# Performance work log

Hardware: AMD Instinct MI355X
Metric: run time of the kernel (lower is better)

The kernel has to match this reference:

```python
import jax, jax.numpy as jnp
import numpy as np
import math

B, T = 32768, 34
VOCAB = 14
SQRT_HD = math.sqrt(3.0)

def _pos_flat_index():
    # flatten (source, index) pairs into indices of a [14,3] table:
    # rows 0-9 = digit spiral enc, row 10 = z10_enc, rows 11-13 = special_enc
    flat = []
    for p in range(34):
        if p < 10:
            flat.append(p)
        elif p == 10:
            flat.append(11 + 0)
        elif p < 21:
            flat.append(p - 11)
        elif p == 21:
            flat.append(11 + 1)
        elif p < 33:
            z = p - 22
            flat.append(z if z < 10 else 10)
        else:
            flat.append(11 + 2)
    return np.array(flat, dtype=np.int32)

POS_FLAT = _pos_flat_index()

def setup_inputs() -> dict:
    key = jax.random.key(0)
    ks = jax.random.split(key, 12)
    r = lambda k, s: jax.random.normal(k, s, dtype=jnp.float32)
    return {
        'idx': jax.random.randint(ks[0], (B, T), 0, VOCAB, dtype=jnp.int64),
        'tok_emb': r(ks[1], (14, 3)),
        'pos_params': r(ks[2], (4,)),
        'z10_enc': r(ks[3], (1, 3)),
        'special_enc': r(ks[4], (3, 3)),
        'wq': r(ks[5], (3, 6)), 'wk': r(ks[6], (3, 6)), 'wv': r(ks[7], (3, 6)),
        'wo': r(ks[8], (6, 6)),
        'ln1_g': jnp.ones(6), 'ln1_b': jnp.zeros(6),
        'ln2_g': jnp.ones(6), 'ln2_b': jnp.zeros(6),
        'lnf_g': jnp.ones(6), 'lnf_b': jnp.zeros(6),
        'ffn_w1': r(ks[9], (6, 2)), 'ffn_b1': jnp.zeros(2),
        'ffn_w2': r(ks[10], (2, 6)), 'ffn_b2': jnp.zeros(6),
        'head_w': r(ks[11], (6, 3)),
    }

def _ln(x, g, b):
    mu = x.mean(-1, keepdims=True)
    var = ((x - mu) ** 2).mean(-1, keepdims=True)
    return (x - mu) * jax.lax.rsqrt(var + 1e-5) * g + b

def _forward(idx, tok_emb, pos_params, z10_enc, special_enc, wq, wk, wv, wo,
             ln1_g, ln1_b, ln2_g, ln2_b, lnf_g, lnf_b,
             ffn_w1, ffn_b1, ffn_w2, ffn_b2, head_w):
    amp, phase, slope, offset = pos_params[0], pos_params[1], pos_params[2], pos_params[3]
    i = jnp.arange(10, dtype=jnp.float32)
    ang = 2.0 * math.pi * i / 10.0 + phase
    digit = jnp.stack([amp * jnp.cos(ang), amp * jnp.sin(ang), slope * i + offset], -1)  # [10,3]
    table = jnp.concatenate([digit, z10_enc, special_enc], 0)  # [14,3]
    Tn = idx.shape[1]
    pos = table[POS_FLAT][:Tn]  # [T,3]
    tok = tok_emb[idx]  # [B,T,3]
    x = jnp.concatenate([tok, jnp.broadcast_to(pos, tok.shape)], -1)  # [B,T,6]
    h = _ln(x, ln1_g, ln1_b)
    h_tok, h_pos = h[..., :3], h[..., 3:]
    Bn = idx.shape[0]
    q = (h_pos @ wq).reshape(Bn, Tn, 2, 3)
    k = (h_pos @ wk).reshape(Bn, Tn, 2, 3)
    v = (h_tok @ wv).reshape(Bn, Tn, 2, 3)
    attn = jnp.einsum('bqhd,bkhd->bhqk', q, k) / SQRT_HD
    mask = jnp.tril(jnp.ones((Tn, Tn), bool))
    attn = jax.nn.softmax(jnp.where(mask, attn, -jnp.inf), axis=-1)
    o = jnp.einsum('bhqk,bkhd->bqhd', attn, v).reshape(Bn, Tn, 6)
    x = x + o @ wo
    h2 = _ln(x, ln2_g, ln2_b)
    x = x + (jax.nn.gelu(h2 @ ffn_w1 + ffn_b1, approximate=False) @ ffn_w2 + ffn_b2)
    x = _ln(x, lnf_g, lnf_b)
    return (x @ head_w) @ tok_emb.T  # [B,T,14]

def reference(idx, tok_emb, pos_params, z10_enc, special_enc, wq, wk, wv, wo,
              ln1_g, ln1_b, ln2_g, ln2_b, lnf_g, lnf_b,
              ffn_w1, ffn_b1, ffn_w2, ffn_b2, head_w):
    return _forward(idx, tok_emb, pos_params, z10_enc, special_enc, wq, wk, wv, wo,
                    ln1_g, ln1_b, ln2_g, ln2_b, lnf_g, lnf_b,
                    ffn_w1, ffn_b1, ffn_w2, ffn_b2, head_w)
```

## Files before the change

### kernel.cpp

```cpp
#include <hip/hip_runtime.h>
#include <math.h>

#define BT    34
#define TPR   17
#define RPB   15
#define BLOCK 256

typedef float v2f __attribute__((ext_vector_type(2)));
typedef float v4f __attribute__((ext_vector_type(4)));

#define QSCALE 0.83294037332470f

#if __has_builtin(__builtin_amdgcn_exp2f)
#define EXP2(x) __builtin_amdgcn_exp2f(x)
#else
#define EXP2(x) exp2f(x)
#endif

__device__ __forceinline__ void ln6n(const v2f* x, v2f* o) {
  v2f mu = (x[0]+x[1]+x[2]+x[3]+x[4]+x[5]) * (1.0f/6.0f);
  v2f v = (v2f){0.f, 0.f};
  #pragma unroll
  for (int c = 0; c < 6; ++c) { v2f d = x[c]-mu; v += d*d; }
  v2f inv = (v2f){ rsqrtf(v.x*(1.0f/6.0f) + 1e-5f),
                   rsqrtf(v.y*(1.0f/6.0f) + 1e-5f) };
  #pragma unroll
  for (int c = 0; c < 6; ++c) o[c] = (x[c]-mu)*inv;
}

__global__ __launch_bounds__(BLOCK, 5)
void addtrans_kernel(const int* __restrict__ idx,
                     const float* __restrict__ tok_emb,
                     const float* __restrict__ pos_params,
                     const float* __restrict__ z10_enc,
                     const float* __restrict__ special_enc,
                     const float* __restrict__ wq,
                     const float* __restrict__ wk,
                     const float* __restrict__ wv,
                     const float* __restrict__ wo,
                     const float* __restrict__ ln1_g, const float* __restrict__ ln1_b,
                     const float* __restrict__ ln2_g, const float* __restrict__ ln2_b,
                     const float* __restrict__ lnf_g, const float* __restrict__ lnf_b,
                     const float* __restrict__ ffn_w1, const float* __restrict__ ffn_b1,
                     const float* __restrict__ ffn_w2, const float* __restrict__ ffn_b2,
                     const float* __restrict__ head_w,
                     float* __restrict__ out, int B)
{
  __shared__ __align__(16) float s_mem[RPB*BT*14];
  __shared__ int   s_idx[RPB*BT];
  __shared__ float s_te[42];
  __shared__ float s_pos[BT*3];
  __shared__ float s_wqf[18], s_wkf[18], s_wvf[18];
  __shared__ float s_qb[6], s_kb[6], s_vb[6];
  __shared__ float s_wo[36];
  __shared__ float s_w1f[12], s_fb1f[2];
  __shared__ float s_w2[12], s_fb2[6];
  __shared__ float s_hwf[18], s_yb[3];

  const int tid = threadIdx.x;
  const int b0  = blockIdx.x * RPB;

  if (tid < 42) s_te[tid] = tok_emb[tid];
  if (tid < 18) {
    const int r = tid / 6;
    s_wqf[tid] = wq[tid] * ln1_g[3+r];
    s_wkf[tid] = wk[tid] * ln1_g[3+r];
    s_wvf[tid] = wv[tid] * ln1_g[r];
    s_hwf[tid] = head_w[tid] * lnf_g[tid/3];
  }
  if (tid < 36) s_wo[tid] = wo[tid];
  if (tid < 12) { s_w1f[tid] = ffn_w1[tid] * ln2_g[tid>>1]; s_w2[tid] = ffn_w2[tid]; }
  if (tid < 6)  {
    s_qb[tid] = ln1_b[3]*wq[tid] + ln1_b[4]*wq[6+tid] + ln1_b[5]*wq[12+tid];
    s_kb[tid] = ln1_b[3]*wk[tid] + ln1_b[4]*wk[6+tid] + ln1_b[5]*wk[12+tid];
    s_vb[tid] = ln1_b[0]*wv[tid] + ln1_b[1]*wv[6+tid] + ln1_b[2]*wv[12+tid];
    s_fb2[tid] = ffn_b2[tid];
  }
  if (tid < 3) {
    float a = 0.f;
    #pragma unroll
    for (int c = 0; c < 6; ++c) a += lnf_b[c]*head_w[c*3+tid];
    s_yb[tid] = a;
  }
  if (tid < 2) {
    float a = ffn_b1[tid];
    #pragma unroll
    for (int d = 0; d < 6; ++d) a += ln2_b[d]*ffn_w1[d*2+tid];
    s_fb1f[tid] = a;
  }
  {
    int nr = B - b0; if (nr > RPB) nr = RPB;
    const int tot = nr * BT;
    for (int i = tid; i < tot; i += BLOCK) s_idx[i] = idx[b0*BT + i];
  }
  if (tid < BT) {
    int p = tid, f;
    if (p < 10) f = p;
    else if (p == 10) f = 11;
    else if (p < 21) f = p - 11;
    else if (p == 21) f = 12;
    else if (p < 33) { int z = p - 22; f = (z < 10) ? z : 10; }
    else f = 13;
    float e0, e1, e2;
    if (f < 10) {
      float amp = pos_params[0], ph = pos_params[1], sl = pos_params[2], of = pos_params[3];
      float ang = 0.62831853071795864769f * (float)f + ph;
      e0 = amp * cosf(ang); e1 = amp * sinf(ang); e2 = sl * (float)f + of;
    } else if (f == 10) { e0 = z10_enc[0]; e1 = z10_enc[1]; e2 = z10_enc[2]; }
    else { int u = f - 11; e0 = special_enc[u*3]; e1 = special_enc[u*3+1]; e2 = special_enc[u*3+2]; }
    s_pos[tid*3+0] = e0; s_pos[tid*3+1] = e1; s_pos[tid*3+2] = e2;
  }
  __syncthreads();

  const int row = tid % RPB;
  const int j   = tid / RPB;
  const int b   = b0 + row;
  const bool active = (j < TPR) && (b < B);

  v2f qpA[3], qpB[3];
  v2f x6[6];

  if (active) {
    const int tA = j, tB = j + TPR;
    const int vA = s_idx[row*BT + tA];
    const int vB = s_idx[row*BT + tB];
    #pragma unroll
    for (int c = 0; c < 3; ++c) {
      x6[c]   = (v2f){ s_te[vA*3+c],  s_te[vB*3+c]  };
      x6[3+c] = (v2f){ s_pos[tA*3+c], s_pos[tB*3+c] };
    }
    v2f h[6];
    ln6n(x6, h);
    v2f q6[6], k6[6], v6[6];
    #pragma unroll
    for (int c = 0; c < 6; ++c) {
      q6[c] = (v2f){s_qb[c], s_qb[c]} + h[3]*s_wqf[c] + h[4]*s_wqf[6+c] + h[5]*s_wqf[12+c];
      k6[c] = (v2f){s_kb[c], s_kb[c]} + h[3]*s_wkf[c] + h[4]*s_wkf[6+c] + h[5]*s_wkf[12+c];
      v6[c] = (v2f){s_vb[c], s_vb[c]} + h[0]*s_wvf[c] + h[1]*s_wvf[6+c] + h[2]*s_wvf[12+c];
    }
    #pragma unroll
    for (int d = 0; d < 3; ++d) {
      qpA[d] = (v2f){ q6[d].x, q6[3+d].x } * QSCALE;
      qpB[d] = (v2f){ q6[d].y, q6[3+d].y } * QSCALE;
    }
    v4f* pA = (v4f*)&s_mem[(tA*RPB + row)*12];
    pA[0] = (v4f){ k6[0].x, k6[3].x, k6[1].x, k6[4].x };
    pA[1] = (v4f){ k6[2].x, k6[5].x, v6[0].x, v6[3].x };
    pA[2] = (v4f){ v6[1].x, v6[4].x, v6[2].x, v6[5].x };
    v4f* pB = (v4f*)&s_mem[(tB*RPB + row)*12];
    pB[0] = (v4f){ k6[0].y, k6[3].y, k6[1].y, k6[4].y };
    pB[1] = (v4f){ k6[2].y, k6[5].y, v6[0].y, v6[3].y };
    pB[2] = (v4f){ v6[1].y, v6[4].y, v6[2].y, v6[5].y };
  }
  __syncthreads();

  v2f l0 = (v2f){0.f,0.f}, l1 = (v2f){0.f,0.f};
  v2f o0[3] = {(v2f){0.f,0.f},(v2f){0.f,0.f},(v2f){0.f,0.f}};
  v2f o1[3] = {(v2f){0.f,0.f},(v2f){0.f,0.f},(v2f){0.f,0.f}};
  if (active) {
    const float* kvbase = s_mem + row*12;
    v4f A  = ((const v4f*)kvbase)[0];
    v4f Bv = ((const v4f*)kvbase)[1];
    v4f C  = ((const v4f*)kvbase)[2];
    for (int k = 0; k <= j; ++k) {
      const v4f Ac = A, Bc = Bv, Cc = C;
      const v4f* nxt = (const v4f*)(kvbase + (k+1)*(RPB*12));
      A = nxt[0]; Bv = nxt[1]; C = nxt[2];
      v2f kA = (v2f){Ac.x, Ac.y}, kB = (v2f){Ac.z, Ac.w}, kC = (v2f){Bc.x, Bc.y};
      v2f vA = (v2f){Bc.z, Bc.w}, vB = (v2f){Cc.x, Cc.y}, vC = (v2f){Cc.z, Cc.w};
      v2f s0 = qpA[0]*kA + qpA[1]*kB + qpA[2]*kC;
      v2f p0 = (v2f){EXP2(s0.x), EXP2(s0.y)};
      l0 += p0; o0[0] += p0*vA; o0[1] += p0*vB; o0[2] += p0*vC;
      v2f s1 = qpB[0]*kA + qpB[1]*kB + qpB[2]*kC;
      v2f p1 = (v2f){EXP2(s1.x), EXP2(s1.y)};
      l1 += p1; o1[0] += p1*vA; o1[1] += p1*vB; o1[2] += p1*vC;
    }
    #pragma unroll 4
    for (int i = 1; i <= TPR; ++i) {
      const int k = j + i;
      const v4f Ac = A, Bc = Bv, Cc = C;
      const v4f* nxt = (const v4f*)(kvbase + (k+1)*(RPB*12));
      A = nxt[0]; Bv = nxt[1]; C = nxt[2];
      v2f kA = (v2f){Ac.x, Ac.y}, kB = (v2f){Ac.z, Ac.w}, kC = (v2f){Bc.x, Bc.y};
      v2f vA = (v2f){Bc.z, Bc.w}, vB = (v2f){Cc.x, Cc.y}, vC = (v2f){Cc.z, Cc.w};
      v2f s1 = qpB[0]*kA + qpB[1]*kB + qpB[2]*kC;
      v2f p1 = (v2f){EXP2(s1.x), EXP2(s1.y)};
      l1 += p1; o1[0] += p1*vA; o1[1] += p1*vB; o1[2] += p1*vC;
    }
  }
  __syncthreads();

  if (active) {
    const float rA0 = __builtin_amdgcn_rcpf(l0.x);
    const float rA1 = __builtin_amdgcn_rcpf(l0.y);
    const float rB0 = __builtin_amdgcn_rcpf(l1.x);
    const float rB1 = __builtin_amdgcn_rcpf(l1.y);
    v2f a6[6];
    a6[0] = (v2f){ o0[0].x*rA0, o1[0].x*rB0 };
    a6[1] = (v2f){ o0[1].x*rA0, o1[1].x*rB0 };
    a6[2] = (v2f){ o0[2].x*rA0, o1[2].x*rB0 };
    a6[3] = (v2f){ o0[0].y*rA1, o1[0].y*rB1 };
    a6[4] = (v2f){ o0[1].y*rA1, o1[1].y*rB1 };
    a6[5] = (v2f){ o0[2].y*rA1, o1[2].y*rB1 };
    v2f xn[6];
    #pragma unroll
    for (int c = 0; c < 6; ++c) {
      xn[c] = x6[c]
            + a6[0]*s_wo[c]    + a6[1]*s_wo[6+c]  + a6[2]*s_wo[12+c]
            + a6[3]*s_wo[18+c] + a6[4]*s_wo[24+c] + a6[5]*s_wo[30+c];
    }
    v2f t2[6];
    ln6n(xn, t2);
    v2f a0 = (v2f){s_fb1f[0], s_fb1f[0]};
    v2f a1 = (v2f){s_fb1f[1], s_fb1f[1]};
    #pragma unroll
    for (int d = 0; d < 6; ++d) { a0 += t2[d]*s_w1f[d*2]; a1 += t2[d]*s_w1f[d*2+1]; }
    const float KIS2 = 0.70710678118654752440f;
    v2f g0 = (v2f){ 0.5f*a0.x*(1.0f + erff(a0.x*KIS2)),
                    0.5f*a0.y*(1.0f + erff(a0.y*KIS2)) };
    v2f g1 = (v2f){ 0.5f*a1.x*(1.0f + erff(a1.x*KIS2)),
                    0.5f*a1.y*(1.0f + erff(a1.y*KIS2)) };
    #pragma unroll
    for (int c = 0; c < 6; ++c) xn[c] += g0*s_w2[c] + g1*s_w2[6+c] + s_fb2[c];
    v2f tf[6];
    ln6n(xn, tf);
    v2f y0 = (v2f){s_yb[0], s_yb[0]};
    v2f y1 = (v2f){s_yb[1], s_yb[1]};
    v2f y2 = (v2f){s_yb[2], s_yb[2]};
    #pragma unroll
    for (int c = 0; c < 6; ++c) {
      y0 += tf[c]*s_hwf[c*3+0]; y1 += tf[c]*s_hwf[c*3+1]; y2 += tf[c]*s_hwf[c*3+2];
    }
    v2f* lpA = (v2f*)&s_mem[(row*BT + j      )*14];
    v2f* lpB = (v2f*)&s_mem[(row*BT + j + TPR)*14];
    #pragma unroll
    for (int u = 0; u < 7; ++u) {
      const int c0 = 2*u, c1 = 2*u+1;
      v2f lg0 = y0*s_te[c0*3+0] + y1*s_te[c0*3+1] + y2*s_te[c0*3+2];
      v2f lg1 = y0*s_te[c1*3+0] + y1*s_te[c1*3+1] + y2*s_te[c1*3+2];
      lpA[u] = (v2f){ lg0.x, lg1.x };
      lpB[u] = (v2f){ lg0.y, lg1.y };
    }
  }
  __syncthreads();

  {
    int nrows = B - b0; if (nrows > RPB) nrows = RPB;
    if (nrows > 0) {
      const int n4 = nrows * (BT*14/4);
      v4f* dst = reinterpret_cast<v4f*>(out + (size_t)b0 * (BT*14));
      const v4f* src = reinterpret_cast<const v4f*>(s_mem);
      for (int i = tid; i < n4; i += BLOCK)
        __builtin_nontemporal_store(src[i], dst + i);
    }
  }
}

extern "C" void kernel_launch(void* const* d_in, const int* in_sizes, int n_in,
                              void* d_out, int out_size, void* d_ws, size_t ws_size,
                              hipStream_t stream) {
  const int B = in_sizes[0] / BT;
  const int grid = (B + RPB - 1) / RPB;
  addtrans_kernel<<<grid, BLOCK, 0, stream>>>(
      (const int*)d_in[0],   (const float*)d_in[1], (const float*)d_in[2],
      (const float*)d_in[3], (const float*)d_in[4], (const float*)d_in[5],
      (const float*)d_in[6], (const float*)d_in[7], (const float*)d_in[8],
      (const float*)d_in[9], (const float*)d_in[10], (const float*)d_in[11],
      (const float*)d_in[12], (const float*)d_in[13], (const float*)d_in[14],
      (const float*)d_in[15], (const float*)d_in[16], (const float*)d_in[17],
      (const float*)d_in[18], (const float*)d_in[19],
      (float*)d_out, B);
}
```

Baseline: 133.9 us.

## Make causal attention loops wave-uniform with masking and pad embedding tables

The per-thread causal loops, whose trip counts depend on each lane's query position, are replaced by wave-uniform loops. A readfirstlane-derived minimum position sets a shared bound, the second loop is fully unrolled, and out-of-range keys are zeroed with a multiplicative mask, which removes divergent loop control. Token and position embeddings are padded to 4 floats so each lookup is a single vector LDS load. The unused tail of shared memory is zeroed so masked reads past the valid K/V region stay finite. The cost is some redundant exp/FMA work on masked keys, and correctness depends on the assumption that lanes in one wave span at most 5 query positions.

Result: slower. 136.7 us (+2.1%).

```diff
diff --git a/kernel.cpp b/kernel.cpp
--- a/kernel.cpp
+++ b/kernel.cpp
@@ -48,8 +48,8 @@
 {
   __shared__ __align__(16) float s_mem[RPB*BT*14];
   __shared__ int   s_idx[RPB*BT];
-  __shared__ float s_te[42];
-  __shared__ float s_pos[BT*3];
+  __shared__ __align__(16) float s_te4[14*4];
+  __shared__ __align__(16) float s_pos4[BT*4];
   __shared__ float s_wqf[18], s_wkf[18], s_wvf[18];
   __shared__ float s_qb[6], s_kb[6], s_vb[6];
   __shared__ float s_wo[36];
@@ -60,7 +60,8 @@
   const int tid = threadIdx.x;
   const int b0  = blockIdx.x * RPB;
 
-  if (tid < 42) s_te[tid] = tok_emb[tid];
+  if (tid < 255) *(v4f*)&s_mem[RPB*BT*12 + tid*4] = (v4f){0.f,0.f,0.f,0.f};
+  if (tid < 56) s_te4[tid] = ((tid & 3) < 3) ? tok_emb[(tid >> 2)*3 + (tid & 3)] : 0.f;
   if (tid < 18) {
     const int r = tid / 6;
     s_wqf[tid] = wq[tid] * ln1_g[3+r];
@@ -108,7 +109,7 @@
       e0 = amp * cosf(ang); e1 = amp * sinf(ang); e2 = sl * (float)f + of;
     } else if (f == 10) { e0 = z10_enc[0]; e1 = z10_enc[1]; e2 = z10_enc[2]; }
     else { int u = f - 11; e0 = special_enc[u*3]; e1 = special_enc[u*3+1]; e2 = special_enc[u*3+2]; }
-    s_pos[tid*3+0] = e0; s_pos[tid*3+1] = e1; s_pos[tid*3+2] = e2;
+    s_pos4[tid*4+0] = e0; s_pos4[tid*4+1] = e1; s_pos4[tid*4+2] = e2; s_pos4[tid*4+3] = 0.f;
   }
   __syncthreads();
 
@@ -124,11 +125,12 @@
     const int tA = j, tB = j + TPR;
     const int vA = s_idx[row*BT + tA];
     const int vB = s_idx[row*BT + tB];
-    #pragma unroll
-    for (int c = 0; c < 3; ++c) {
-      x6[c]   = (v2f){ s_te[vA*3+c],  s_te[vB*3+c]  };
-      x6[3+c] = (v2f){ s_pos[tA*3+c], s_pos[tB*3+c] };
-    }
+    v4f teA = *(const v4f*)&s_te4[vA*4];
+    v4f teB = *(const v4f*)&s_te4[vB*4];
+    v4f poA = *(const v4f*)&s_pos4[tA*4];
+    v4f poB = *(const v4f*)&s_pos4[tB*4];
+    x6[0] = (v2f){teA.x, teB.x}; x6[1] = (v2f){teA.y, teB.y}; x6[2] = (v2f){teA.z, teB.z};
+    x6[3] = (v2f){poA.x, poB.x}; x6[4] = (v2f){poA.y, poB.y}; x6[5] = (v2f){poA.z, poB.z};
     v2f h[6];
     ln6n(x6, h);
     v2f q6[6], k6[6], v6[6];
@@ -158,33 +160,36 @@
   v2f o0[3] = {(v2f){0.f,0.f},(v2f){0.f,0.f},(v2f){0.f,0.f}};
   v2f o1[3] = {(v2f){0.f,0.f},(v2f){0.f,0.f},(v2f){0.f,0.f}};
   if (active) {
-    const float* kvbase = s_mem + row*12;
-    v4f A  = ((const v4f*)kvbase)[0];
-    v4f Bv = ((const v4f*)kvbase)[1];
-    v4f C  = ((const v4f*)kvbase)[2];
-    for (int k = 0; k <= j; ++k) {
-      const v4f Ac = A, Bc = Bv, Cc = C;
-      const v4f* nxt = (const v4f*)(kvbase + (k+1)*(RPB*12));
-      A = nxt[0]; Bv = nxt[1]; C = nxt[2];
+    const int jmin = __builtin_amdgcn_readfirstlane(j);
+    const int dj   = j - jmin;
+    __builtin_assume(dj >= 0 && dj <= 4);
+    const float* kvr = s_mem + row*12;
+
+    const int t1max = jmin + 4;
+    for (int t = 0; t <= t1max; ++t) {
+      const v4f* p = (const v4f*)(kvr + t*(RPB*12));
+      v4f Ac = p[0], Bc = p[1], Cc = p[2];
       v2f kA = (v2f){Ac.x, Ac.y}, kB = (v2f){Ac.z, Ac.w}, kC = (v2f){Bc.x, Bc.y};
       v2f vA = (v2f){Bc.z, Bc.w}, vB = (v2f){Cc.x, Cc.y}, vC = (v2f){Cc.z, Cc.w};
       v2f s0 = qpA[0]*kA + qpA[1]*kB + qpA[2]*kC;
-      v2f p0 = (v2f){EXP2(s0.x), EXP2(s0.y)};
+      const float mA = (t <= j) ? 1.f : 0.f;
+      v2f p0 = (v2f){EXP2(s0.x), EXP2(s0.y)} * mA;
       l0 += p0; o0[0] += p0*vA; o0[1] += p0*vB; o0[2] += p0*vC;
       v2f s1 = qpB[0]*kA + qpB[1]*kB + qpB[2]*kC;
       v2f p1 = (v2f){EXP2(s1.x), EXP2(s1.y)};
       l1 += p1; o1[0] += p1*vA; o1[1] += p1*vB; o1[2] += p1*vC;
     }
-    #pragma unroll 4
-    for (int i = 1; i <= TPR; ++i) {
-      const int k = j + i;
-      const v4f Ac = A, Bc = Bv, Cc = C;
-      const v4f* nxt = (const v4f*)(kvbase + (k+1)*(RPB*12));
-      A = nxt[0]; Bv = nxt[1]; C = nxt[2];
+
+    const float* kvw = s_mem + jmin*(RPB*12) + row*12;
+    #pragma unroll
+    for (int tt = 5; tt <= 21; ++tt) {
+      const v4f* p = (const v4f*)(kvw + tt*(RPB*12));
+      v4f Ac = p[0], Bc = p[1], Cc = p[2];
       v2f kA = (v2f){Ac.x, Ac.y}, kB = (v2f){Ac.z, Ac.w}, kC = (v2f){Bc.x, Bc.y};
       v2f vA = (v2f){Bc.z, Bc.w}, vB = (v2f){Cc.x, Cc.y}, vC = (v2f){Cc.z, Cc.w};
       v2f s1 = qpB[0]*kA + qpB[1]*kB + qpB[2]*kC;
-      v2f p1 = (v2f){EXP2(s1.x), EXP2(s1.y)};
+      const float mB = (tt <= dj + 17) ? 1.f : 0.f;
+      v2f p1 = (v2f){EXP2(s1.x), EXP2(s1.y)} * mB;
       l1 += p1; o1[0] += p1*vA; o1[1] += p1*vB; o1[2] += p1*vC;
     }
   }
@@ -229,15 +234,18 @@
     v2f y2 = (v2f){s_yb[2], s_yb[2]};
     #pragma unroll
     for (int c = 0; c < 6; ++c) {
+      const v4f hw = *(const v4f*)&s_hwf[0] ;
+      (void)hw;
       y0 += tf[c]*s_hwf[c*3+0]; y1 += tf[c]*s_hwf[c*3+1]; y2 += tf[c]*s_hwf[c*3+2];
     }
     v2f* lpA = (v2f*)&s_mem[(row*BT + j      )*14];
     v2f* lpB = (v2f*)&s_mem[(row*BT + j + TPR)*14];
     #pragma unroll
     for (int u = 0; u < 7; ++u) {
-      const int c0 = 2*u, c1 = 2*u+1;
-      v2f lg0 = y0*s_te[c0*3+0] + y1*s_te[c0*3+1] + y2*s_te[c0*3+2];
-      v2f lg1 = y0*s_te[c1*3+0] + y1*s_te[c1*3+1] + y2*s_te[c1*3+2];
+      v4f t0 = *(const v4f*)&s_te4[(2*u  )*4];
+      v4f t1 = *(const v4f*)&s_te4[(2*u+1)*4];
+      v2f lg0 = y0*t0.x + y1*t0.y + y2*t0.z;
+      v2f lg1 = y0*t1.x + y1*t1.y + y2*t1.z;
       lpA[u] = (v2f){ lg0.x, lg1.x };
       lpB[u] = (v2f){ lg0.y, lg1.y };
     }
```

## Halve output staging LDS and read token ids directly to raise occupancy

Applied to the files above, without the earlier changes.

The shared-memory output staging buffer is shrunk so it reuses the key/value region. Logits are written and flushed in two phases: rows 0-7 first, then rows 8-14. The shared idx buffer is removed, so each thread reads its two token ids straight from global memory. Launch bounds are raised from 5 to 8 so more blocks can be resident per CU. The trade-off is two extra block barriers and tighter register limits, which could cause spills.

Result: no change. 133.9 us (+0.0%).

```diff
diff --git a/kernel.cpp b/kernel.cpp
--- a/kernel.cpp
+++ b/kernel.cpp
@@ -28,7 +28,7 @@
   for (int c = 0; c < 6; ++c) o[c] = (x[c]-mu)*inv;
 }
 
-__global__ __launch_bounds__(BLOCK, 5)
+__global__ __launch_bounds__(BLOCK, 8)
 void addtrans_kernel(const int* __restrict__ idx,
                      const float* __restrict__ tok_emb,
                      const float* __restrict__ pos_params,
@@ -46,8 +46,7 @@
                      const float* __restrict__ head_w,
                      float* __restrict__ out, int B)
 {
-  __shared__ __align__(16) float s_mem[RPB*BT*14];
-  __shared__ int   s_idx[RPB*BT];
+  __shared__ __align__(16) float s_mem[RPB*BT*12 + 180];
   __shared__ float s_te[42];
   __shared__ float s_pos[BT*3];
   __shared__ float s_wqf[18], s_wkf[18], s_wvf[18];
@@ -87,11 +86,6 @@
     #pragma unroll
     for (int d = 0; d < 6; ++d) a += ln2_b[d]*ffn_w1[d*2+tid];
     s_fb1f[tid] = a;
-  }
-  {
-    int nr = B - b0; if (nr > RPB) nr = RPB;
-    const int tot = nr * BT;
-    for (int i = tid; i < tot; i += BLOCK) s_idx[i] = idx[b0*BT + i];
   }
   if (tid < BT) {
     int p = tid, f;
@@ -122,8 +116,8 @@
 
   if (active) {
     const int tA = j, tB = j + TPR;
-    const int vA = s_idx[row*BT + tA];
-    const int vB = s_idx[row*BT + tB];
+    const int vA = idx[b*BT + tA];
+    const int vB = idx[b*BT + tB];
     #pragma unroll
     for (int c = 0; c < 3; ++c) {
       x6[c]   = (v2f){ s_te[vA*3+c],  s_te[vB*3+c]  };
@@ -190,6 +184,7 @@
   }
   __syncthreads();
 
+  v2f yl0 = (v2f){0.f,0.f}, yl1 = (v2f){0.f,0.f}, yl2 = (v2f){0.f,0.f};
   if (active) {
     const float rA0 = __builtin_amdgcn_rcpf(l0.x);
     const float rA1 = __builtin_amdgcn_rcpf(l0.y);
@@ -224,31 +219,60 @@
     for (int c = 0; c < 6; ++c) xn[c] += g0*s_w2[c] + g1*s_w2[6+c] + s_fb2[c];
     v2f tf[6];
     ln6n(xn, tf);
-    v2f y0 = (v2f){s_yb[0], s_yb[0]};
-    v2f y1 = (v2f){s_yb[1], s_yb[1]};
-    v2f y2 = (v2f){s_yb[2], s_yb[2]};
+    yl0 = (v2f){s_yb[0], s_yb[0]};
+    yl1 = (v2f){s_yb[1], s_yb[1]};
+    yl2 = (v2f){s_yb[2], s_yb[2]};
     #pragma unroll
     for (int c = 0; c < 6; ++c) {
-      y0 += tf[c]*s_hwf[c*3+0]; y1 += tf[c]*s_hwf[c*3+1]; y2 += tf[c]*s_hwf[c*3+2];
-    }
+      yl0 += tf[c]*s_hwf[c*3+0]; yl1 += tf[c]*s_hwf[c*3+1]; yl2 += tf[c]*s_hwf[c*3+2];
+    }
+  }
+
+  if (active && row < 8) {
     v2f* lpA = (v2f*)&s_mem[(row*BT + j      )*14];
     v2f* lpB = (v2f*)&s_mem[(row*BT + j + TPR)*14];
     #pragma unroll
     for (int u = 0; u < 7; ++u) {
       const int c0 = 2*u, c1 = 2*u+1;
-      v2f lg0 = y0*s_te[c0*3+0] + y1*s_te[c0*3+1] + y2*s_te[c0*3+2];
-      v2f lg1 = y0*s_te[c1*3+0] + y1*s_te[c1*3+1] + y2*s_te[c1*3+2];
+      v2f lg0 = yl0*s_te[c0*3+0] + yl1*s_te[c0*3+1] + yl2*s_te[c0*3+2];
+      v2f lg1 = yl0*s_te[c1*3+0] + yl1*s_te[c1*3+1] + yl2*s_te[c1*3+2];
       lpA[u] = (v2f){ lg0.x, lg1.x };
       lpB[u] = (v2f){ lg0.y, lg1.y };
     }
   }
   __syncthreads();
-
   {
     int nrows = B - b0; if (nrows > RPB) nrows = RPB;
-    if (nrows > 0) {
-      const int n4 = nrows * (BT*14/4);
+    int nr0 = nrows < 8 ? nrows : 8;
+    if (nr0 > 0) {
+      const int n4 = nr0 * (BT*14/4);
       v4f* dst = reinterpret_cast<v4f*>(out + (size_t)b0 * (BT*14));
+      const v4f* src = reinterpret_cast<const v4f*>(s_mem);
+      for (int i = tid; i < n4; i += BLOCK)
+        __builtin_nontemporal_store(src[i], dst + i);
+    }
+  }
+  __syncthreads();
+
+  if (active && row >= 8) {
+    v2f* lpA = (v2f*)&s_mem[((row-8)*BT + j      )*14];
+    v2f* lpB = (v2f*)&s_mem[((row-8)*BT + j + TPR)*14];
+    #pragma unroll
+    for (int u = 0; u < 7; ++u) {
+      const int c0 = 2*u, c1 = 2*u+1;
+      v2f lg0 = yl0*s_te[c0*3+0] + yl1*s_te[c0*3+1] + yl2*s_te[c0*3+2];
+      v2f lg1 = yl0*s_te[c1*3+0] + yl1*s_te[c1*3+1] + yl2*s_te[c1*3+2];
+      lpA[u] = (v2f){ lg0.x, lg1.x };
+      lpB[u] = (v2f){ lg0.y, lg1.y };
+    }
+  }
+  __syncthreads();
+  {
+    int nrows = B - b0; if (nrows > RPB) nrows = RPB;
+    int nr1 = nrows - 8;
+    if (nr1 > 0) {
+      const int n4 = nr1 * (BT*14/4);
+      v4f* dst = reinterpret_cast<v4f*>(out + ((size_t)b0 + 8) * (BT*14));
       const v4f* src = reinterpret_cast<const v4f*>(s_mem);
       for (int i = tid; i < n4; i += BLOCK)
         __builtin_nontemporal_store(src[i], dst + i);
```
